# Kernel tuning notes

Hardware: AMD Instinct MI355X
Metric: run time of the kernel (lower is better)

## Reference

```python
import jax, jax.numpy as jnp
import numpy as np

B, T, N, HID, ATTN = 32, 64, 128, 128, 128

def setup_inputs() -> dict:
    key = jax.random.key(0)
    ks = jax.random.split(key, 7)
    s_h = 1.0 / np.sqrt(HID)
    return {
        "cur_h": jax.random.normal(ks[0], (B, HID), jnp.float32),
        "history_h": jax.random.normal(ks[1], (B, T, N, HID), jnp.float32),
        "Wx_w": jax.random.uniform(ks[2], (ATTN, HID), jnp.float32, -s_h, s_h),
        "Wx_b": jax.random.uniform(ks[3], (ATTN,), jnp.float32, -s_h, s_h),
        "Wh_w": jax.random.uniform(ks[4], (ATTN, HID), jnp.float32, -s_h, s_h),
        "Wh_b": jax.random.uniform(ks[5], (ATTN,), jnp.float32, -s_h, s_h),
        "v_w": jax.random.uniform(ks[6], (ATTN,), jnp.float32, -1.0 / np.sqrt(ATTN), 1.0 / np.sqrt(ATTN)),
    }

def reference(cur_h, history_h, Wx_w, Wx_b, Wh_w, Wh_b, v_w):
    # history projection: [B,T,N,A]
    hist_proj = jnp.einsum("btnh,ah->btna", history_h, Wh_w) + Wh_b
    # current projection broadcast over (T,N): [B,1,1,A]
    cur_proj = (cur_h @ Wx_w.T + Wx_b)[:, None, None, :]
    # additive score: v . tanh(...) -> [B,T,N]
    score = jnp.einsum("btna,a->btn", jnp.tanh(hist_proj + cur_proj), v_w)
    Bv = history_h.shape[0]
    score_flat = score.reshape(Bv, -1)                      # [B, T*N]
    attn = jax.nn.softmax(score_flat, axis=1)               # softmax over all history positions
    hist_flat = history_h.reshape(Bv, -1, history_h.shape[-1])  # [B, T*N, H]
    attn_h = jnp.einsum("bs,bsh->bh", attn, hist_flat)
    return cur_h + attn_h
```

## Files before the change

### kernel.cpp

```cpp
#include <hip/hip_runtime.h>
#include <hip/hip_bf16.h>

#define BB     32
#define HIDD   128
#define ATT    128
#define SS     8192
#define BLKPB  32
#define PART_STRIDE 132

typedef float f32x4 __attribute__((ext_vector_type(4)));
typedef short s16x8 __attribute__((ext_vector_type(8)));

__device__ inline unsigned short f2bf(float x) {
    unsigned u = __float_as_uint(x);
    u += 0x7FFFu + ((u >> 16) & 1u);
    return (unsigned short)(u >> 16);
}
__device__ inline float bf2f(unsigned short h) {
    return __uint_as_float(((unsigned)h) << 16);
}
__device__ inline float fast_tanh(float x) {
    x = fminf(15.f, fmaxf(-15.f, x));
    float e2 = __expf(2.f * x);
    return (e2 - 1.f) * __builtin_amdgcn_rcpf(e2 + 1.f);
}
__device__ inline unsigned cvt_pk_bf16(float a, float b) {
    unsigned r;
    asm("v_cvt_pk_bf16_f32 %0, %1, %2" : "=v"(r) : "v"(a), "v"(b));
    return r;
}

__global__ void prep_kernel(const float* __restrict__ whw,
                            unsigned short* __restrict__ wbf,
                            const float* __restrict__ cur,
                            const float* __restrict__ wxw,
                            const float* __restrict__ wxb,
                            const float* __restrict__ whb,
                            float* __restrict__ bias2) {
    if (blockIdx.x < 64) {
        int i = blockIdx.x * 256 + threadIdx.x;
        wbf[i] = f2bf(whw[i]);
    } else {
        __shared__ float sc[HIDD];
        int b = blockIdx.x - 64;
        int a = threadIdx.x;
        if (a < HIDD) sc[a] = cur[b * HIDD + a];
        __syncthreads();
        if (a < ATT) {
            float d = 0.f;
#pragma unroll 8
            for (int h = 0; h < HIDD; ++h) d += sc[h] * wxw[a * HIDD + h];
            bias2[b * ATT + a] = d + wxb[a] + whb[a];
        }
    }
}

__global__ __launch_bounds__(256, 2) void attn_main_kernel(
    const float* __restrict__ hist,
    const unsigned short* __restrict__ wbf,
    const float* __restrict__ bias2,
    const float* __restrict__ vw,
    float* __restrict__ partials)
{
    __shared__ __align__(16) unsigned short sW[ATT * HIDD];
    __shared__ float sB[ATT];
    __shared__ float sV[ATT];
    __shared__ float sAccW[4][HIDD];
    __shared__ float sML[4][2];

    const int tid  = threadIdx.x;
    const int bid  = blockIdx.x;
    const int b    = bid >> 5;
    const int blk  = bid & 31;
    const int lane = tid & 63;
    const int wid  = tid >> 6;
    const int l15  = lane & 15;
    const int lg   = lane >> 4;

    const float* srcw = hist + ((size_t)b * SS + (size_t)blk * 256 + wid * 64) * HIDD;

    f32x4 raw[8];
    auto issue = [&](int t) {
        const float* r = srcw + (size_t)(t * 16 + l15) * HIDD + lg * 8;
#pragma unroll
        for (int kk = 0; kk < 4; ++kk) {
            raw[2 * kk]     = *(const f32x4*)(r + kk * 32);
            raw[2 * kk + 1] = *(const f32x4*)(r + kk * 32 + 4);
        }
        __builtin_amdgcn_sched_barrier(0);
    };

    issue(0);

#pragma unroll
    for (int i = 0; i < 8; ++i) {
        int e = (i * 256 + tid) * 8;
        int row = e >> 7;
        s16x8 v = *(const s16x8*)(wbf + e);
        *(s16x8*)&sW[e ^ ((row & 7) << 3)] = v;
    }
    if (tid < ATT) { sB[tid] = bias2[b * ATT + tid]; sV[tid] = vw[tid]; }
    __syncthreads();

    float m_run = -1e30f, l_run = 0.f;
    f32x4 acc[8];
#pragma unroll
    for (int q = 0; q < 8; ++q) acc[q] = (f32x4){0.f, 0.f, 0.f, 0.f};

#pragma unroll
    for (int t = 0; t < 4; ++t) {
        s16x8 hfrag[4];
#pragma unroll
        for (int kk = 0; kk < 4; ++kk) {
            union { s16x8 v; unsigned w[4]; } fr;
            fr.w[0] = cvt_pk_bf16(raw[2 * kk].x,     raw[2 * kk].y);
            fr.w[1] = cvt_pk_bf16(raw[2 * kk].z,     raw[2 * kk].w);
            fr.w[2] = cvt_pk_bf16(raw[2 * kk + 1].x, raw[2 * kk + 1].y);
            fr.w[3] = cvt_pk_bf16(raw[2 * kk + 1].z, raw[2 * kk + 1].w);
            hfrag[kk] = fr.v;
        }
        if (t < 3) issue(t + 1);

        float p = 0.f;
#pragma unroll
        for (int at = 0; at < 8; ++at) {
            s16x8 wfrag[4];
#pragma unroll
            for (int kk = 0; kk < 4; ++kk) {
                int idx = ((at * 16 + l15) * HIDD + kk * 32 + lg * 8) ^ ((l15 & 7) << 3);
                wfrag[kk] = *(const s16x8*)&sW[idx];
            }
            f32x4 d = {0.f, 0.f, 0.f, 0.f};
#pragma unroll
            for (int kk = 0; kk < 4; ++kk)
                d = __builtin_amdgcn_mfma_f32_16x16x32_bf16(wfrag[kk], hfrag[kk], d, 0, 0, 0);
            f32x4 bb = *(const f32x4*)&sB[at * 16 + lg * 4];
            f32x4 vx = *(const f32x4*)&sV[at * 16 + lg * 4];
#pragma unroll
            for (int r = 0; r < 4; ++r)
                p += vx[r] * fast_tanh(d[r] + bb[r]);
        }
        p += __shfl_xor(p, 16, 64);
        p += __shfl_xor(p, 32, 64);

        float mx = p;
#pragma unroll
        for (int m = 1; m < 16; m <<= 1) mx = fmaxf(mx, __shfl_xor(mx, m, 64));
        float m_new = fmaxf(m_run, mx);
        float so = __expf(m_run - m_new);
        float ev = __expf(p - m_new);
        float es = ev;
#pragma unroll
        for (int m = 1; m < 16; m <<= 1) es += __shfl_xor(es, m, 64);
        l_run = l_run * so + es;
        m_run = m_new;

#pragma unroll
        for (int q = 0; q < 8; ++q) acc[q] *= so;
#pragma unroll
        for (int kk = 0; kk < 4; ++kk) {
            union { s16x8 v; unsigned short u[8]; } fr; fr.v = hfrag[kk];
#pragma unroll
            for (int i = 0; i < 4; ++i) acc[2 * kk][i]     += ev * bf2f(fr.u[i]);
#pragma unroll
            for (int i = 0; i < 4; ++i) acc[2 * kk + 1][i] += ev * bf2f(fr.u[4 + i]);
        }
    }

#pragma unroll
    for (int m = 1; m < 16; m <<= 1) {
#pragma unroll
        for (int q = 0; q < 8; ++q) {
#pragma unroll
            for (int i = 0; i < 4; ++i)
                acc[q][i] += __shfl_xor(acc[q][i], m, 64);
        }
    }
    if (l15 == 0) {
#pragma unroll
        for (int kk = 0; kk < 4; ++kk) {
            *(f32x4*)&sAccW[wid][kk * 32 + lg * 8]     = acc[2 * kk];
            *(f32x4*)&sAccW[wid][kk * 32 + lg * 8 + 4] = acc[2 * kk + 1];
        }
    }
    if (lane == 0) { sML[wid][0] = m_run; sML[wid][1] = l_run; }
    __syncthreads();

    if (tid < HIDD) {
        float M = fmaxf(fmaxf(sML[0][0], sML[1][0]), fmaxf(sML[2][0], sML[3][0]));
        float num = 0.f, den = 0.f;
#pragma unroll
        for (int w = 0; w < 4; ++w) {
            float sc = __expf(sML[w][0] - M);
            den += sML[w][1] * sc;
            num += sAccW[w][tid] * sc;
        }
        float* part = partials + (size_t)(b * BLKPB + blk) * PART_STRIDE;
        part[4 + tid] = num;
        if (tid == 0) { part[0] = M; part[1] = den; }
    }
}

__global__ void attn_combine_kernel(const float* __restrict__ cur,
                                    const float* __restrict__ partials,
                                    float* __restrict__ out)
{
    int b = blockIdx.x, h = threadIdx.x;
    const float* pb = partials + (size_t)b * BLKPB * PART_STRIDE;
    float M = -INFINITY;
    for (int c = 0; c < BLKPB; ++c) M = fmaxf(M, pb[c * PART_STRIDE]);
    float num = 0.f, den = 0.f;
    for (int c = 0; c < BLKPB; ++c) {
        float scale = __expf(pb[c * PART_STRIDE] - M);
        den += pb[c * PART_STRIDE + 1] * scale;
        num += pb[c * PART_STRIDE + 4 + h] * scale;
    }
    out[b * HIDD + h] = cur[b * HIDD + h] + num / den;
}

extern "C" void kernel_launch(void* const* d_in, const int* in_sizes, int n_in,
                              void* d_out, int out_size, void* d_ws, size_t ws_size,
                              hipStream_t stream) {
    const float* cur  = (const float*)d_in[0];
    const float* hist = (const float*)d_in[1];
    const float* wxw  = (const float*)d_in[2];
    const float* wxb  = (const float*)d_in[3];
    const float* whw  = (const float*)d_in[4];
    const float* whb  = (const float*)d_in[5];
    const float* vw   = (const float*)d_in[6];
    float* out = (float*)d_out;

    unsigned short* wbf = (unsigned short*)d_ws;
    float* bias2    = (float*)((char*)d_ws + 32768);
    float* partials = (float*)((char*)d_ws + 32768 + 16384);

    prep_kernel<<<96, 256, 0, stream>>>(whw, wbf, cur, wxw, wxb, whb, bias2);
    attn_main_kernel<<<BB * BLKPB, 256, 0, stream>>>(hist, wbf, bias2, vw, partials);
    attn_combine_kernel<<<BB, HIDD, 0, stream>>>(cur, partials, out);
}
```

Baseline: 47.17 us.

## Fuse prep, main and combine kernels into one with last-block reduction

Removes the separate prep and combine kernels. Each main block now converts Wh to bf16 itself, computes its batch's current projection bias, and uses an atomic counter so the last block per batch does the softmax combine and writes the output. This saves two kernel launches and their serialization gaps, at the cost of redundant weight conversion and bias GEMV in every block, plus a memset for the counters.

```diff
diff --git a/kernel.cpp b/kernel.cpp
--- a/kernel.cpp
+++ b/kernel.cpp
@@ -7,15 +7,11 @@
 #define SS     8192
 #define BLKPB  32
 #define PART_STRIDE 132
+#define PART_BYTES (BB * BLKPB * PART_STRIDE * 4)
 
 typedef float f32x4 __attribute__((ext_vector_type(4)));
 typedef short s16x8 __attribute__((ext_vector_type(8)));
 
-__device__ inline unsigned short f2bf(float x) {
-    unsigned u = __float_as_uint(x);
-    u += 0x7FFFu + ((u >> 16) & 1u);
-    return (unsigned short)(u >> 16);
-}
 __device__ inline float bf2f(unsigned short h) {
     return __uint_as_float(((unsigned)h) << 16);
 }
@@ -30,43 +26,26 @@
     return r;
 }
 
-__global__ void prep_kernel(const float* __restrict__ whw,
-                            unsigned short* __restrict__ wbf,
-                            const float* __restrict__ cur,
-                            const float* __restrict__ wxw,
-                            const float* __restrict__ wxb,
-                            const float* __restrict__ whb,
-                            float* __restrict__ bias2) {
-    if (blockIdx.x < 64) {
-        int i = blockIdx.x * 256 + threadIdx.x;
-        wbf[i] = f2bf(whw[i]);
-    } else {
-        __shared__ float sc[HIDD];
-        int b = blockIdx.x - 64;
-        int a = threadIdx.x;
-        if (a < HIDD) sc[a] = cur[b * HIDD + a];
-        __syncthreads();
-        if (a < ATT) {
-            float d = 0.f;
-#pragma unroll 8
-            for (int h = 0; h < HIDD; ++h) d += sc[h] * wxw[a * HIDD + h];
-            bias2[b * ATT + a] = d + wxb[a] + whb[a];
-        }
-    }
-}
-
-__global__ __launch_bounds__(256, 2) void attn_main_kernel(
+__global__ __launch_bounds__(256, 2) void attn_fused_kernel(
     const float* __restrict__ hist,
-    const unsigned short* __restrict__ wbf,
-    const float* __restrict__ bias2,
+    const float* __restrict__ cur,
+    const float* __restrict__ whw,
+    const float* __restrict__ wxw,
+    const float* __restrict__ wxb,
+    const float* __restrict__ whb,
     const float* __restrict__ vw,
-    float* __restrict__ partials)
+    float* __restrict__ partials,
+    int* __restrict__ cnt,
+    float* __restrict__ out)
 {
     __shared__ __align__(16) unsigned short sW[ATT * HIDD];
     __shared__ float sB[ATT];
     __shared__ float sV[ATT];
+    __shared__ float sC[HIDD];
+    __shared__ float sBp[2][ATT];
     __shared__ float sAccW[4][HIDD];
     __shared__ float sML[4][2];
+    __shared__ int   sLast;
 
     const int tid  = threadIdx.x;
     const int bid  = blockIdx.x;
@@ -96,10 +75,31 @@
     for (int i = 0; i < 8; ++i) {
         int e = (i * 256 + tid) * 8;
         int row = e >> 7;
-        s16x8 v = *(const s16x8*)(wbf + e);
-        *(s16x8*)&sW[e ^ ((row & 7) << 3)] = v;
-    }
-    if (tid < ATT) { sB[tid] = bias2[b * ATT + tid]; sV[tid] = vw[tid]; }
+        f32x4 w0 = *(const f32x4*)(whw + e);
+        f32x4 w1 = *(const f32x4*)(whw + e + 4);
+        union { s16x8 v; unsigned w[4]; } o;
+        o.w[0] = cvt_pk_bf16(w0.x, w0.y);
+        o.w[1] = cvt_pk_bf16(w0.z, w0.w);
+        o.w[2] = cvt_pk_bf16(w1.x, w1.y);
+        o.w[3] = cvt_pk_bf16(w1.z, w1.w);
+        *(s16x8*)&sW[e ^ ((row & 7) << 3)] = o.v;
+    }
+    if (tid < HIDD) { sC[tid] = cur[b * HIDD + tid]; sV[tid] = vw[tid]; }
+    __syncthreads();
+
+    {
+        const int a = tid & 127, half = tid >> 7;
+        float d = 0.f;
+#pragma unroll
+        for (int hh = 0; hh < 16; ++hh) {
+            f32x4 x = *(const f32x4*)(wxw + a * HIDD + half * 64 + hh * 4);
+            f32x4 c = *(const f32x4*)&sC[half * 64 + hh * 4];
+            d += x.x * c.x + x.y * c.y + x.z * c.z + x.w * c.w;
+        }
+        sBp[half][a] = d;
+    }
+    __syncthreads();
+    if (tid < ATT) sB[tid] = sBp[0][tid] + sBp[1][tid] + wxb[tid] + whb[tid];
     __syncthreads();
 
     float m_run = -1e30f, l_run = 0.f;
@@ -186,6 +186,7 @@
     if (lane == 0) { sML[wid][0] = m_run; sML[wid][1] = l_run; }
     __syncthreads();
 
+    float* part = partials + (size_t)(b * BLKPB + blk) * PART_STRIDE;
     if (tid < HIDD) {
         float M = fmaxf(fmaxf(sML[0][0], sML[1][0]), fmaxf(sML[2][0], sML[3][0]));
         float num = 0.f, den = 0.f;
@@ -195,27 +196,29 @@
             den += sML[w][1] * sc;
             num += sAccW[w][tid] * sc;
         }
-        float* part = partials + (size_t)(b * BLKPB + blk) * PART_STRIDE;
         part[4 + tid] = num;
         if (tid == 0) { part[0] = M; part[1] = den; }
     }
-}
-
-__global__ void attn_combine_kernel(const float* __restrict__ cur,
-                                    const float* __restrict__ partials,
-                                    float* __restrict__ out)
-{
-    int b = blockIdx.x, h = threadIdx.x;
-    const float* pb = partials + (size_t)b * BLKPB * PART_STRIDE;
-    float M = -INFINITY;
-    for (int c = 0; c < BLKPB; ++c) M = fmaxf(M, pb[c * PART_STRIDE]);
-    float num = 0.f, den = 0.f;
-    for (int c = 0; c < BLKPB; ++c) {
-        float scale = __expf(pb[c * PART_STRIDE] - M);
-        den += pb[c * PART_STRIDE + 1] * scale;
-        num += pb[c * PART_STRIDE + 4 + h] * scale;
-    }
-    out[b * HIDD + h] = cur[b * HIDD + h] + num / den;
+
+    __threadfence();
+    __syncthreads();
+    if (tid == 0) sLast = (atomicAdd(&cnt[b], 1) == BLKPB - 1) ? 1 : 0;
+    __syncthreads();
+    if (sLast && tid < HIDD) {
+        __threadfence();
+        const float* pb = partials + (size_t)b * BLKPB * PART_STRIDE;
+        float M = -INFINITY;
+#pragma unroll 8
+        for (int c = 0; c < BLKPB; ++c) M = fmaxf(M, pb[c * PART_STRIDE]);
+        float num = 0.f, den = 0.f;
+#pragma unroll 8
+        for (int c = 0; c < BLKPB; ++c) {
+            float scale = __expf(pb[c * PART_STRIDE] - M);
+            den += pb[c * PART_STRIDE + 1] * scale;
+            num += pb[c * PART_STRIDE + 4 + tid] * scale;
+        }
+        out[b * HIDD + tid] = sC[tid] + num / den;
+    }
 }
 
 extern "C" void kernel_launch(void* const* d_in, const int* in_sizes, int n_in,
@@ -230,11 +233,10 @@
     const float* vw   = (const float*)d_in[6];
     float* out = (float*)d_out;
 
-    unsigned short* wbf = (unsigned short*)d_ws;
-    float* bias2    = (float*)((char*)d_ws + 32768);
-    float* partials = (float*)((char*)d_ws + 32768 + 16384);
-
-    prep_kernel<<<96, 256, 0, stream>>>(whw, wbf, cur, wxw, wxb, whb, bias2);
-    attn_main_kernel<<<BB * BLKPB, 256, 0, stream>>>(hist, wbf, bias2, vw, partials);
-    attn_combine_kernel<<<BB, HIDD, 0, stream>>>(cur, partials, out);
-}
+    float* partials = (float*)d_ws;
+    int*   cnt      = (int*)((char*)d_ws + PART_BYTES);
+
+    hipMemsetAsync(cnt, 0, BB * sizeof(int), stream);
+    attn_fused_kernel<<<BB * BLKPB, 256, 0, stream>>>(
+        hist, cur, whw, wxw, wxb, whb, vw, partials, cnt, out);
+}
```

Result: slower. 154.4 us (+227.3%).
